# Kernel optimization log

Measured on AMD Instinct MI355X. Metric: run time of the kernel, lower is better.

The kernel has to match this reference:

```python
import jax, jax.numpy as jnp
import numpy as np
from jax.scipy.special import logsumexp

B, T, V, E, H, K = 64, 512, 21128, 256, 512, 31


def setup_inputs() -> dict:
    key = jax.random.key(0)
    ks = jax.random.split(key, 32)
    s = 1.0 / np.sqrt(H)

    def u(k, shape):
        return jax.random.uniform(k, shape, jnp.float32, -s, s)

    inp = {
        "input_ids": jax.random.randint(ks[0], (B, T), 0, V),
        "labels": jax.random.randint(ks[1], (B, T), 0, K),
        "emb": jax.random.normal(ks[2], (V, E), jnp.float32) * 0.05,
    }
    i = 3
    for layer, insz in (("l0", E), ("l1", 2 * H)):
        for d in ("f", "b"):
            inp["w_ih_%s%s" % (layer, d)] = u(ks[i], (3 * H, insz)); i += 1
            inp["w_hh_%s%s" % (layer, d)] = u(ks[i], (3 * H, H)); i += 1
            inp["b_ih_%s%s" % (layer, d)] = u(ks[i], (3 * H,)); i += 1
            inp["b_hh_%s%s" % (layer, d)] = u(ks[i], (3 * H,)); i += 1
    inp["cls_w"] = u(ks[i], (K, 2 * H))
    inp["cls_b"] = u(ks[i + 1], (K,))
    inp["crf_start"] = jax.random.normal(ks[i + 2], (K,), jnp.float32) * 0.1
    inp["crf_end"] = jax.random.normal(ks[i + 3], (K,), jnp.float32) * 0.1
    inp["crf_trans"] = jax.random.normal(ks[i + 4], (K, K), jnp.float32) * 0.1
    return inp


def gru_dir(x, w_ih, w_hh, b_ih, b_hh, reverse):
    # x: [B, T, in]. PyTorch GRU gate math, gates ordered (r, z, n).
    xp = jnp.einsum('bti,gi->btg', x, w_ih) + b_ih  # [B, T, 3H] precomputed input gates
    if reverse:
        xp = xp[:, ::-1]
    h0 = jnp.zeros((x.shape[0], w_hh.shape[1]), x.dtype)

    def step(h, xt):
        gh = h @ w_hh.T + b_hh
        xr, xz, xn = jnp.split(xt, 3, axis=-1)
        hr, hz, hn = jnp.split(gh, 3, axis=-1)
        r = jax.nn.sigmoid(xr + hr)
        z = jax.nn.sigmoid(xz + hz)
        n = jnp.tanh(xn + r * hn)
        h_new = (1.0 - z) * n + z * h
        return h_new, h_new

    _, hs = jax.lax.scan(step, h0, jnp.swapaxes(xp, 0, 1))
    hs = jnp.swapaxes(hs, 0, 1)  # [B, T, H]
    if reverse:
        hs = hs[:, ::-1]
    return hs


def crf_llh(emissions, tags, mask, start, end, trans):
    # Linear-chain CRF log-likelihood, summed over batch. mask[:, 0] assumed True.
    Bn = emissions.shape[0]
    mf = mask.astype(emissions.dtype)
    bidx = jnp.arange(Bn)
    em_t = jnp.take_along_axis(emissions, tags[:, :, None], axis=2)[:, :, 0]  # [B, T]
    num = start[tags[:, 0]] + em_t[:, 0]
    tr = trans[tags[:, :-1], tags[:, 1:]]  # [B, T-1]
    num = num + jnp.sum((tr + em_t[:, 1:]) * mf[:, 1:], axis=1)
    last_idx = jnp.sum(mask.astype(jnp.int32), axis=1) - 1
    num = num + end[tags[bidx, last_idx]]

    alpha0 = start[None, :] + emissions[:, 0]  # [B, K]

    def step(alpha, inp):
        em, m = inp  # em [B, K], m [B]
        nxt = logsumexp(alpha[:, :, None] + trans[None] + em[:, None, :], axis=1)
        return jnp.where(m[:, None], nxt, alpha), None

    alpha, _ = jax.lax.scan(
        step, alpha0,
        (jnp.swapaxes(emissions[:, 1:], 0, 1), jnp.swapaxes(mask[:, 1:], 0, 1)))
    denom = logsumexp(alpha + end[None, :], axis=1)
    return jnp.sum(num - denom)


def reference(input_ids, labels, emb,
              w_ih_l0f, w_hh_l0f, b_ih_l0f, b_hh_l0f,
              w_ih_l0b, w_hh_l0b, b_ih_l0b, b_hh_l0b,
              w_ih_l1f, w_hh_l1f, b_ih_l1f, b_hh_l1f,
              w_ih_l1b, w_hh_l1b, b_ih_l1b, b_hh_l1b,
              cls_w, cls_b, crf_start, crf_end, crf_trans):
    x = emb[input_ids]  # [B, T, E]
    f0 = gru_dir(x, w_ih_l0f, w_hh_l0f, b_ih_l0f, b_hh_l0f, False)
    b0 = gru_dir(x, w_ih_l0b, w_hh_l0b, b_ih_l0b, b_hh_l0b, True)
    h1 = jnp.concatenate([f0, b0], axis=-1)  # [B, T, 2H]
    f1 = gru_dir(h1, w_ih_l1f, w_hh_l1f, b_ih_l1f, b_hh_l1f, False)
    b1 = gru_dir(h1, w_ih_l1b, w_hh_l1b, b_ih_l1b, b_hh_l1b, True)
    gru_out = jnp.concatenate([f1, b1], axis=-1)  # [B, T, 2H]
    emissions = jnp.einsum('bth,kh->btk', gru_out, cls_w) + cls_b  # [B, T, K]
    mask = labels > -1  # labels.gt(labels_padding_value=-1)
    loss = -crf_llh(emissions, labels, mask, crf_start, crf_end, crf_trans)
    return (loss, emissions)
```

## Files before the change

kernel.cpp:

```cpp
#include <hip/hip_runtime.h>

#define DI __device__ __forceinline__

constexpr int B_  = 64;
constexpr int T_  = 512;
constexpr int E_  = 256;
constexpr int H_  = 512;
constexpr int G_  = 1536;
constexpr int H2_ = 1024;
constexpr int K_  = 31;
constexpr int BT_ = B_ * T_;
constexpr int TC_ = 64;
constexpr int NC_ = T_ / TC_;

typedef float        f32x4  __attribute__((ext_vector_type(4)));
typedef short        bf16x8 __attribute__((ext_vector_type(8)));
typedef unsigned int u32x4  __attribute__((ext_vector_type(4)));
typedef unsigned long long ull;

DI float bf2f(unsigned short u) {
    union { unsigned int i; float f; } v; v.i = ((unsigned int)u) << 16; return v.f;
}
DI unsigned short f2bf(float f) {
    union { float f; unsigned int i; } v; v.f = f;
    unsigned int r = v.i + 0x7fffu + ((v.i >> 16) & 1u);
    return (unsigned short)(r >> 16);
}
DI float sigm(float x) { return 1.f / (1.f + __expf(-x)); }
DI float tanh_(float x) {
    x = fminf(15.f, fmaxf(-15.f, x));
    float e = __expf(-2.f * x);
    return (1.f - e) / (1.f + e);
}

#define MFMA16(a, b, c) __builtin_amdgcn_mfma_f32_16x16x32_bf16(a, b, c, 0, 0, 0)

__global__ __launch_bounds__(256) void cvt_cls(const float* __restrict__ src,
                                               unsigned short* __restrict__ dstf,
                                               unsigned short* __restrict__ dstb) {
    int i = blockIdx.x * 256 + threadIdx.x;
    if (i >= 32 * H_) return;
    int n = i >> 9, k = i & 511;
    float vf = (n < K_) ? src[n * H2_ + k] : 0.f;
    float vb = (n < K_) ? src[n * H2_ + H_ + k] : 0.f;
    dstf[i] = f2bf(vf);
    dstb[i] = f2bf(vb);
}

__global__ __launch_bounds__(256) void emis_bias_init(const float* __restrict__ cls_b,
                                                      float* __restrict__ out1) {
    int i = blockIdx.x * 256 + threadIdx.x;
    int stride = gridDim.x * 256;
    for (; i < BT_ * K_; i += stride) {
        int n = i - (i / K_) * K_;
        out1[i] = cls_b[n];
    }
}

template <bool OUTF32, bool ACCUM, bool WF32, bool AGATHER>
DI void gemm_tile(unsigned short (*As)[40], unsigned short (*Ws)[40],
                  const unsigned short* A, const float* gsrc, const int* ids, int lda,
                  size_t arow0, const void* W, int ldw, int nrows, int n0,
                  const float* bias, void* Cout, int ldc, size_t crow0,
                  int nout, int ksz, int tid) {
    const int w = tid >> 6, l = tid & 63;
    const int srow = tid >> 2, sc8 = (tid & 3) * 8;
    const int mw = (w >> 1) * 32, nw = (w & 1) * 32;
    const int fl = l & 15, fk = (l >> 4) * 8;
    f32x4 z4 = { 0.f, 0.f, 0.f, 0.f };
    f32x4 acc[2][2];
    acc[0][0] = z4; acc[0][1] = z4; acc[1][0] = z4; acc[1][1] = z4;
    size_t abase;
    if (AGATHER) abase = (size_t)ids[arow0 + srow] * lda;
    else         abase = (arow0 + srow) * (size_t)lda;

    for (int kc = 0; kc < ksz; kc += 32) {
        u32x4 av, wvv;
        if (AGATHER) {
            const float4* ap = (const float4*)(gsrc + abase + kc + sc8);
            float4 a0 = ap[0], a1 = ap[1];
            union { unsigned short s[8]; u32x4 v; } r;
            r.s[0] = f2bf(a0.x); r.s[1] = f2bf(a0.y); r.s[2] = f2bf(a0.z); r.s[3] = f2bf(a0.w);
            r.s[4] = f2bf(a1.x); r.s[5] = f2bf(a1.y); r.s[6] = f2bf(a1.z); r.s[7] = f2bf(a1.w);
            av = r.v;
        } else {
            av = *(const u32x4*)(A + abase + kc + sc8);
        }
        if (WF32) {
            const float4* wp = (const float4*)((const float*)W + (size_t)(n0 + srow) * ldw + kc + sc8);
            float4 w0 = wp[0], w1 = wp[1];
            union { unsigned short s[8]; u32x4 v; } r;
            r.s[0] = f2bf(w0.x); r.s[1] = f2bf(w0.y); r.s[2] = f2bf(w0.z); r.s[3] = f2bf(w0.w);
            r.s[4] = f2bf(w1.x); r.s[5] = f2bf(w1.y); r.s[6] = f2bf(w1.z); r.s[7] = f2bf(w1.w);
            wvv = r.v;
        } else {
            if (n0 + srow < nrows)
                wvv = *(const u32x4*)((const unsigned short*)W + (size_t)(n0 + srow) * ldw + kc + sc8);
            else { u32x4 zz = { 0u, 0u, 0u, 0u }; wvv = zz; }
        }
        __syncthreads();
        *(u32x4*)&As[srow][sc8] = av;
        *(u32x4*)&Ws[srow][sc8] = wvv;
        __syncthreads();
        bf16x8 a0 = *(const bf16x8*)&As[mw + fl][fk];
        bf16x8 a1 = *(const bf16x8*)&As[mw + 16 + fl][fk];
        bf16x8 b0 = *(const bf16x8*)&Ws[nw + fl][fk];
        bf16x8 b1 = *(const bf16x8*)&Ws[nw + 16 + fl][fk];
        acc[0][0] = MFMA16(a0, b0, acc[0][0]);
        acc[0][1] = MFMA16(a0, b1, acc[0][1]);
        acc[1][0] = MFMA16(a1, b0, acc[1][0]);
        acc[1][1] = MFMA16(a1, b1, acc[1][1]);
    }

    #pragma unroll
    for (int mf = 0; mf < 2; ++mf)
        #pragma unroll
        for (int nf = 0; nf < 2; ++nf) {
            int col = n0 + nw + nf * 16 + fl;
            if (col >= nout) continue;
            float bv = bias ? bias[col] : 0.f;
            #pragma unroll
            for (int j = 0; j < 4; ++j) {
                int r = mw + mf * 16 + (l >> 4) * 4 + j;
                size_t crow = crow0 + r;
                float v = acc[mf][nf][j] + bv;
                if (OUTF32) {
                    float* C = (float*)Cout;
                    if (ACCUM) C[crow * ldc + col] += v;
                    else       C[crow * ldc + col] = v;
                } else {
                    ((unsigned short*)Cout)[crow * ldc + col] = f2bf(v);
                }
            }
        }
}

template <bool OUTF32, bool ACCUM, bool WF32, bool AGATHER>
__global__ __launch_bounds__(256) void gemm_k(
        const unsigned short* __restrict__ A, const float* __restrict__ gsrc,
        const int* __restrict__ ids, int lda, int m_base, int astride,
        const void* __restrict__ W, int ldw, int nrows,
        const float* __restrict__ bias,
        void* __restrict__ Cout, int ldc, int c_base, int cstride, int nout, int ksz) {
    __shared__ unsigned short As[64][40];
    __shared__ unsigned short Ws[64][40];
    gemm_tile<OUTF32, ACCUM, WF32, AGATHER>(As, Ws, A, gsrc, ids, lda,
        (size_t)m_base + (size_t)blockIdx.x * astride, W, ldw, nrows,
        blockIdx.y * 64, bias, Cout, ldc,
        (size_t)c_base + (size_t)blockIdx.x * cstride, nout, ksz, threadIdx.x);
}

template <bool AGATHER>
__global__ __launch_bounds__(256, 1) void fused_scan_gemm(
        int c, int layer,
        const unsigned short* __restrict__ xpc_f, const unsigned short* __restrict__ xpc_b,
        const float* __restrict__ whh_f, const float* __restrict__ whh_b,
        const float* __restrict__ bhh_f, const float* __restrict__ bhh_b,
        unsigned int* __restrict__ hpub,
        float* __restrict__ hcar,
        unsigned short* __restrict__ out_f, unsigned short* __restrict__ out_b,
        int ldo, int mode, int* __restrict__ flags,
        const unsigned short* __restrict__ gA, const float* __restrict__ gsrc,
        const int* __restrict__ gids, int glda,
        const float* __restrict__ gwf, const float* __restrict__ gwb,
        const float* __restrict__ gbf, const float* __restrict__ gbb,
        unsigned short* __restrict__ xpf_nxt, unsigned short* __restrict__ xpb_nxt,
        int t0f_n, int t0b_n, int do_gemm) {
    __shared__ unsigned short As[64][40];
    __shared__ unsigned short Ws[64][40];
    __shared__ unsigned short hs[16 * 512];
    const int bid = blockIdx.x;
    const int tid = threadIdx.x;

    if (bid >= 64) {
        if (!do_gemm) return;
        const int gb = bid - 64;
        for (int job = gb; job < 2 * 64 * 24; job += 192) {
            int dirj = job & 1;
            int rest = job >> 1;
            int mt = rest & 63;
            int nt = rest >> 6;
            const float* gw = dirj ? gwb : gwf;
            const float* gbias = dirj ? gbb : gbf;
            unsigned short* gout = dirj ? xpb_nxt : xpf_nxt;
            int t0 = dirj ? t0b_n : t0f_n;
            gemm_tile<false, false, true, AGATHER>(As, Ws, gA, gsrc, gids, glda,
                (size_t)t0 + (size_t)mt * T_, gw, glda, G_, nt * 64, gbias,
                (void*)gout, G_, (size_t)mt * TC_, G_, glda, tid);
        }
        return;
    }

    const int dir = bid >> 5;
    const int rb  = bid & 31;
    const int ug  = rb >> 2;
    const int bg  = rb & 3;
    const int w = tid >> 6, l = tid & 63;
    const int fl = l & 15, q = l >> 4, fko = q * 8;
    const unsigned short* xp = dir ? xpc_b : xpc_f;
    const float* whh = dir ? whh_b : whh_f;
    const float* bhh = dir ? bhh_b : bhh_f;
    unsigned short* outp = dir ? out_b : out_f;
    int* pollb  = flags + (dir * 4 + bg) * 8 * 32;
    int* myflag = pollb + ug * 32;

    const int u0w = ug * 64 + w * 16;
    bf16x8 wv[3][16];
    #pragma unroll
    for (int g = 0; g < 3; ++g)
        #pragma unroll
        for (int ks = 0; ks < 16; ++ks) {
            const float* wp = whh + (size_t)(g * H_ + u0w + fl) * H_ + ks * 32 + fko;
            float4 w0 = *(const float4*)wp, w1 = *(const float4*)(wp + 4);
            union { unsigned short s[8]; bf16x8 v; } r;
            r.s[0] = f2bf(w0.x); r.s[1] = f2bf(w0.y); r.s[2] = f2bf(w0.z); r.s[3] = f2bf(w0.w);
            r.s[4] = f2bf(w1.x); r.s[5] = f2bf(w1.y); r.s[6] = f2bf(w1.z); r.s[7] = f2bf(w1.w);
            wv[g][ks] = r.v;
        }

    const int u = u0w + fl;
    const float br_ = bhh[u], bz_ = bhh[H_ + u], bn_ = bhh[2 * H_ + u];
    const int mb = bg * 16 + q * 4;
    const int srowl = tid >> 4;
    const int sseg  = tid & 15;

    float hp[4];
    if (c > 0) {
        #pragma unroll
        for (int j = 0; j < 4; ++j) hp[j] = hcar[dir * (B_ * H_) + (mb + j) * H_ + u];
    } else {
        #pragma unroll
        for (int j = 0; j < 4; ++j) hp[j] = 0.f;
    }

    unsigned short xg[3][4];
    auto ldxp = [&](int tl) {
        #pragma unroll
        for (int j = 0; j < 4; ++j) {
            const unsigned short* xb = xp + ((size_t)((mb + j) * TC_ + tl) * G_) + u;
            xg[0][j] = xb[0]; xg[1][j] = xb[H_]; xg[2][j] = xb[2 * H_];
        }
    };
    ldxp(dir ? (TC_ - 1) : 0);

    for (int sl = 0; sl < TC_; ++sl) {
        const int s  = c * TC_ + sl;
        const int gs = layer * T_ + s;
        const int t = dir ? (T_ - 1 - s) : s;
        const int tloc = dir ? (TC_ - 1 - sl) : sl;

        f32x4 z4 = { 0.f, 0.f, 0.f, 0.f };
        f32x4 acc[3];
        acc[0] = z4; acc[1] = z4; acc[2] = z4;

        if (s > 0) {
            if (sl > 0) {
                int v = gs;
                if (l < 8) v = __hip_atomic_load(pollb + l * 32, __ATOMIC_RELAXED, __HIP_MEMORY_SCOPE_AGENT);
                while (!__all(v >= gs)) {
                    __builtin_amdgcn_s_sleep(1);
                    if (l < 8) v = __hip_atomic_load(pollb + l * 32, __ATOMIC_RELAXED, __HIP_MEMORY_SCOPE_AGENT);
                }
                asm volatile("" ::: "memory");
            }
            {
                const ull* src = (const ull*)(hpub
                    + ((size_t)((((s - 1) & 1) * 2 + dir) * B_ + bg * 16 + srowl)) * 256)
                    + sseg * 8;
                ull qv[8];
                #pragma unroll
                for (int i = 0; i < 8; ++i)
                    qv[i] = __hip_atomic_load(src + i, __ATOMIC_RELAXED, __HIP_MEMORY_SCOPE_AGENT);
                char* dst = (char*)hs + srowl * 1024;
                #pragma unroll
                for (int i = 0; i < 4; ++i) {
                    unsigned int byt = (unsigned int)(sseg * 64 + i * 16);
                    byt ^= ((unsigned int)(srowl & 7)) << 4;
                    union { ull qq[2]; u32x4 v4; } pk;
                    pk.qq[0] = qv[2 * i]; pk.qq[1] = qv[2 * i + 1];
                    *(u32x4*)(dst + byt) = pk.v4;
                }
            }
            __syncthreads();
            #pragma unroll
            for (int ks = 0; ks < 16; ++ks) {
                unsigned int byt = (unsigned int)(ks * 64 + q * 16);
                byt ^= ((unsigned int)(fl & 7)) << 4;
                bf16x8 afr = *(const bf16x8*)((const char*)hs + fl * 1024 + byt);
                acc[0] = MFMA16(afr, wv[0][ks], acc[0]);
                acc[1] = MFMA16(afr, wv[1][ks], acc[1]);
                acc[2] = MFMA16(afr, wv[2][ks], acc[2]);
            }
        }

        unsigned short hb16s[4];
        #pragma unroll
        for (int j = 0; j < 4; ++j) {
            float xr = bf2f(xg[0][j]);
            float xz = bf2f(xg[1][j]);
            float xn = bf2f(xg[2][j]);
            float r = sigm(xr + acc[0][j] + br_);
            float z = sigm(xz + acc[1][j] + bz_);
            float nn = tanh_(xn + r * (acc[2][j] + bn_));
            float hv = (1.f - z) * nn + z * hp[j];
            hp[j] = hv;
            hb16s[j] = f2bf(hv);
        }

        unsigned int* hw = hpub + (size_t)((s & 1) * 2 + dir) * (B_ * 256);
        #pragma unroll
        for (int j = 0; j < 4; ++j) {
            unsigned int pv = (unsigned int)(unsigned short)__shfl_xor((int)hb16s[j], 1);
            if ((fl & 1) == 0) {
                unsigned int pk32 = (unsigned int)hb16s[j] | (pv << 16);
                __hip_atomic_store(hw + (size_t)(mb + j) * 256 + (u >> 1), pk32,
                                   __ATOMIC_RELAXED, __HIP_MEMORY_SCOPE_AGENT);
            }
        }
        asm volatile("s_waitcnt vmcnt(0)" ::: "memory");
        __syncthreads();
        if (tid == 0)
            __hip_atomic_store(myflag, gs + 1, __ATOMIC_RELAXED, __HIP_MEMORY_SCOPE_AGENT);

        #pragma unroll
        for (int j = 0; j < 4; ++j) {
            size_t row = mode ? (size_t)((mb + j) * TC_ + tloc) : ((size_t)(mb + j) * T_ + t);
            outp[row * ldo + u] = hb16s[j];
        }
        if (sl < TC_ - 1) ldxp(dir ? (TC_ - 2 - sl) : (sl + 1));
    }

    #pragma unroll
    for (int j = 0; j < 4; ++j) hcar[dir * (B_ * H_) + (mb + j) * H_ + u] = hp[j];
}

__global__ __launch_bounds__(64) void crf_kernel(const float* __restrict__ em,
                                                 const int* __restrict__ labels,
                                                 const float* __restrict__ start,
                                                 const float* __restrict__ endv,
                                                 const float* __restrict__ trans,
                                                 float* __restrict__ partials) {
    __shared__ float tr[32 * 32];
    const int b = blockIdx.x, l = threadIdx.x;
    for (int e2 = l; e2 < 961; e2 += 64) {
        int r = e2 / 31, cc = e2 - r * 31;
        tr[r * 32 + cc] = trans[e2];
    }
    if (l < 32) tr[31 * 32 + l] = 0.f;
    __syncthreads();
    const int* lab = labels + b * T_;
    const float* eb = em + (size_t)b * T_ * K_;

    float part = 0.f, cnt = 0.f;
    for (int t = l; t < T_; t += 64) {
        int lt = lab[t];
        if (lt > -1) {
            cnt += 1.f;
            if (t > 0) part += tr[lab[t - 1] * 32 + lt] + eb[t * K_ + lt];
        }
    }
    #pragma unroll
    for (int o = 32; o; o >>= 1) { part += __shfl_xor(part, o); cnt += __shfl_xor(cnt, o); }
    int lastidx = (int)cnt - 1;
    float num = part + start[lab[0]] + eb[lab[0]] + endv[lab[lastidx]];

    const int jj = l & 31, half = l >> 5;
    const int i0 = half * 16;
    const int ecol = (jj < K_) ? jj : (K_ - 1);
    float a = (jj < K_) ? (start[jj] + eb[jj]) : -3.0e38f;
    for (int t = 1; t < T_; ++t) {
        float tv[16];
        float m = -3.0e38f;
        #pragma unroll
        for (int k = 0; k < 16; ++k) {
            float av = __shfl(a, i0 + k);
            float x = av + tr[(i0 + k) * 32 + jj];
            tv[k] = x;
            m = fmaxf(m, x);
        }
        float ss = 0.f;
        #pragma unroll
        for (int k = 0; k < 16; ++k) ss += __expf(tv[k] - m);
        float m2 = __shfl_xor(m, 32), s2 = __shfl_xor(ss, 32);
        float M = fmaxf(m, m2);
        float S = ss * __expf(m - M) + s2 * __expf(m2 - M);
        float anew = eb[t * K_ + ecol] + M + __logf(S);
        a = ((lab[t] > -1) && (jj < K_)) ? anew : a;
    }
    float v = (jj < K_) ? (a + endv[jj]) : -3.0e38f;
    float m = v;
    #pragma unroll
    for (int o = 32; o; o >>= 1) m = fmaxf(m, __shfl_xor(m, o));
    float ss = (half == 0 && jj < K_) ? __expf(v - m) : 0.f;
    #pragma unroll
    for (int o = 32; o; o >>= 1) ss += __shfl_xor(ss, o);
    if (l == 0) partials[b] = num - (m + __logf(ss));
}

__global__ __launch_bounds__(64) void loss_reduce(const float* __restrict__ partials,
                                                  float* __restrict__ out) {
    float v = partials[threadIdx.x];
    #pragma unroll
    for (int o = 32; o; o >>= 1) v += __shfl_xor(v, o);
    if (threadIdx.x == 0) out[0] = -v;
}

__global__ void sentinel(float* __restrict__ out, float v) { out[0] = -v; }

extern "C" void kernel_launch(void* const* d_in, const int* in_sizes, int n_in,
                              void* d_out, int out_size, void* d_ws, size_t ws_size,
                              hipStream_t stream) {
    const int*   ids      = (const int*)d_in[0];
    const int*   labels   = (const int*)d_in[1];
    const float* emb      = (const float*)d_in[2];
    const float* wih[4]   = { (const float*)d_in[3], (const float*)d_in[7], (const float*)d_in[11], (const float*)d_in[15] };
    const float* whh[4]   = { (const float*)d_in[4], (const float*)d_in[8], (const float*)d_in[12], (const float*)d_in[16] };
    const float* bih[4]   = { (const float*)d_in[5], (const float*)d_in[9], (const float*)d_in[13], (const float*)d_in[17] };
    const float* bhh[4]   = { (const float*)d_in[6], (const float*)d_in[10], (const float*)d_in[14], (const float*)d_in[18] };
    const float* cls_w    = (const float*)d_in[19];
    const float* cls_b    = (const float*)d_in[20];
    const float* c_start  = (const float*)d_in[21];
    const float* c_end    = (const float*)d_in[22];
    const float* c_trans  = (const float*)d_in[23];
    float* out = (float*)d_out;
    float* out1 = out + 1;

    char* p = (char*)d_ws;
    size_t used = 0;
    auto alloc = [&](size_t bytes) -> char* {
        char* r = p;
        size_t a = (bytes + 255) & ~(size_t)255;
        p += a; used += a;
        return r;
    };
    unsigned short* xpF[2]; unsigned short* xpB[2];
    for (int i = 0; i < 2; ++i) {
        xpF[i] = (unsigned short*)alloc((size_t)B_ * TC_ * G_ * 2);
        xpB[i] = (unsigned short*)alloc((size_t)B_ * TC_ * G_ * 2);
    }
    unsigned short* h1   = (unsigned short*)alloc((size_t)BT_ * H2_ * 2);
    unsigned short* gof  = (unsigned short*)alloc((size_t)B_ * TC_ * H_ * 2);
    unsigned short* gob  = (unsigned short*)alloc((size_t)B_ * TC_ * H_ * 2);
    unsigned short* clsf  = (unsigned short*)alloc((size_t)32 * H_ * 2);
    unsigned short* clshb = (unsigned short*)alloc((size_t)32 * H_ * 2);
    unsigned int*   hpub  = (unsigned int*)alloc((size_t)2 * 2 * B_ * 256 * 4);
    float*          hcar  = (float*)alloc((size_t)2 * B_ * H_ * 4);
    float*          partials = (float*)alloc((size_t)B_ * 4);
    int*            flags = (int*)alloc((size_t)2 * 4 * 8 * 32 * 4);

    if (used > ws_size) {
        sentinel<<<dim3(1), dim3(1), 0, stream>>>(out, (float)(ws_size >> 20));
        return;
    }

    hipMemsetAsync(flags, 0, (size_t)2 * 4 * 8 * 32 * 4, stream);
    cvt_cls<<<dim3((32 * H_ + 255) / 256), dim3(256), 0, stream>>>(cls_w, clsf, clshb);
    emis_bias_init<<<dim3(1024), dim3(256), 0, stream>>>(cls_b, out1);

    for (int layer = 0; layer < 2; ++layer) {
        const float* wf  = wih[layer * 2 + 0];
        const float* wb  = wih[layer * 2 + 1];
        const float* bf_ = bih[layer * 2 + 0];
        const float* bb_ = bih[layer * 2 + 1];
        const float* whf = whh[layer * 2 + 0];
        const float* whb = whh[layer * 2 + 1];
        const float* bhf = bhh[layer * 2 + 0];
        const float* bhb = bhh[layer * 2 + 1];

        if (layer == 0) {
            gemm_k<false, false, true, true><<<dim3(64, 24), dim3(256), 0, stream>>>(
                nullptr, emb, ids, E_, 0, T_, wf, E_, G_, bf_, (void*)xpF[0], G_, 0, TC_, G_, E_);
            gemm_k<false, false, true, true><<<dim3(64, 24), dim3(256), 0, stream>>>(
                nullptr, emb, ids, E_, T_ - TC_, T_, wb, E_, G_, bb_, (void*)xpB[0], G_, 0, TC_, G_, E_);
        } else {
            gemm_k<false, false, true, false><<<dim3(64, 24), dim3(256), 0, stream>>>(
                h1, nullptr, nullptr, H2_, 0, T_, wf, H2_, G_, bf_, (void*)xpF[0], G_, 0, TC_, G_, H2_);
            gemm_k<false, false, true, false><<<dim3(64, 24), dim3(256), 0, stream>>>(
                h1, nullptr, nullptr, H2_, T_ - TC_, T_, wb, H2_, G_, bb_, (void*)xpB[0], G_, 0, TC_, G_, H2_);
        }

        for (int c = 0; c < NC_; ++c) {
            int dg = (c + 1 < NC_) ? 1 : 0;
            int t0f_n = (c + 1) * TC_;
            int t0b_n = T_ - (c + 2) * TC_;
            if (layer == 0) {
                fused_scan_gemm<true><<<dim3(256), dim3(256), 0, stream>>>(
                    c, 0, xpF[c & 1], xpB[c & 1], whf, whb, bhf, bhb, hpub, hcar,
                    h1, h1 + H_, H2_, 0, flags,
                    nullptr, emb, ids, E_, wf, wb, bf_, bb_,
                    xpF[(c + 1) & 1], xpB[(c + 1) & 1], t0f_n, t0b_n, dg);
            } else {
                fused_scan_gemm<false><<<dim3(256), dim3(256), 0, stream>>>(
                    c, 1, xpF[c & 1], xpB[c & 1], whf, whb, bhf, bhb, hpub, hcar,
                    gof, gob, H_, 1, flags,
                    h1, nullptr, nullptr, H2_, wf, wb, bf_, bb_,
                    xpF[(c + 1) & 1], xpB[(c + 1) & 1], t0f_n, t0b_n, dg);
                int t0f = c * TC_;
                int t0b = T_ - (c + 1) * TC_;
                gemm_k<true, true, false, false><<<dim3(64, 1), dim3(256), 0, stream>>>(
                    gof, nullptr, nullptr, H_, 0, TC_, clsf, H_, 32, nullptr,
                    (void*)out1, K_, t0f, T_, K_, H_);
                gemm_k<true, true, false, false><<<dim3(64, 1), dim3(256), 0, stream>>>(
                    gob, nullptr, nullptr, H_, 0, TC_, clshb, H_, 32, nullptr,
                    (void*)out1, K_, t0b, T_, K_, H_);
            }
        }
    }

    crf_kernel<<<dim3(B_), dim3(64), 0, stream>>>(out1, labels, c_start, c_end, c_trans, partials);
    loss_reduce<<<dim3(1), dim3(64), 0, stream>>>(partials, out);
}
```

Baseline: 4.572 ms.

## Tag published hidden states with step number and validate on load

Each published pair of bf16 hidden values is widened to 64 bits, with the step index stored in the upper 32 bits. Consumers issue the hidden-state loads before the flag poll completes, then check that every tag matches the expected step and re-load until it does. The aim is to overlap the data fetch with flag waiting and to shorten the critical path of cross-block synchronisation. The cost is double the publish traffic, and the flag polling is still kept. The GEMM side-job loop is also reordered so each block takes a contiguous range of 16 jobs, changing the tile order.

```diff
diff --git a/kernel.cpp b/kernel.cpp
--- a/kernel.cpp
+++ b/kernel.cpp
@@ -156,7 +156,7 @@
         const unsigned short* __restrict__ xpc_f, const unsigned short* __restrict__ xpc_b,
         const float* __restrict__ whh_f, const float* __restrict__ whh_b,
         const float* __restrict__ bhh_f, const float* __restrict__ bhh_b,
-        unsigned int* __restrict__ hpub,
+        ull* __restrict__ hpub,
         float* __restrict__ hcar,
         unsigned short* __restrict__ out_f, unsigned short* __restrict__ out_b,
         int ldo, int mode, int* __restrict__ flags,
@@ -175,11 +175,13 @@
     if (bid >= 64) {
         if (!do_gemm) return;
         const int gb = bid - 64;
-        for (int job = gb; job < 2 * 64 * 24; job += 192) {
-            int dirj = job & 1;
-            int rest = job >> 1;
-            int mt = rest & 63;
-            int nt = rest >> 6;
+        #pragma unroll 1
+        for (int it = 0; it < 16; ++it) {
+            int job = gb * 16 + it;
+            int dirj = job / 1536;
+            int r2 = job - dirj * 1536;
+            int nt = r2 >> 6;
+            int mt = r2 & 63;
             const float* gw = dirj ? gwb : gwf;
             const float* gbias = dirj ? gbb : gbf;
             unsigned short* gout = dirj ? xpb_nxt : xpf_nxt;
@@ -254,6 +256,14 @@
         acc[0] = z4; acc[1] = z4; acc[2] = z4;
 
         if (s > 0) {
+            const ull* src = hpub
+                + ((size_t)((((s - 1) & 1) * 2 + dir) * B_) + bg * 16 + srowl) * 256
+                + sseg * 16;
+            ull qv[16];
+            #pragma unroll
+            for (int i = 0; i < 16; ++i)
+                qv[i] = __hip_atomic_load(src + i, __ATOMIC_RELAXED, __HIP_MEMORY_SCOPE_AGENT);
+
             if (sl > 0) {
                 int v = gs;
                 if (l < 8) v = __hip_atomic_load(pollb + l * 32, __ATOMIC_RELAXED, __HIP_MEMORY_SCOPE_AGENT);
@@ -264,20 +274,30 @@
                 asm volatile("" ::: "memory");
             }
             {
-                const ull* src = (const ull*)(hpub
-                    + ((size_t)((((s - 1) & 1) * 2 + dir) * B_ + bg * 16 + srowl)) * 256)
-                    + sseg * 8;
-                ull qv[8];
+                const unsigned int want = (unsigned int)(gs - 1);
+                bool ok = true;
                 #pragma unroll
-                for (int i = 0; i < 8; ++i)
-                    qv[i] = __hip_atomic_load(src + i, __ATOMIC_RELAXED, __HIP_MEMORY_SCOPE_AGENT);
+                for (int i = 0; i < 16; ++i) ok = ok && ((unsigned int)(qv[i] >> 32) == want);
+                while (!__all(ok)) {
+                    #pragma unroll
+                    for (int i = 0; i < 16; ++i)
+                        qv[i] = __hip_atomic_load(src + i, __ATOMIC_RELAXED, __HIP_MEMORY_SCOPE_AGENT);
+                    ok = true;
+                    #pragma unroll
+                    for (int i = 0; i < 16; ++i) ok = ok && ((unsigned int)(qv[i] >> 32) == want);
+                }
+            }
+            {
                 char* dst = (char*)hs + srowl * 1024;
                 #pragma unroll
                 for (int i = 0; i < 4; ++i) {
                     unsigned int byt = (unsigned int)(sseg * 64 + i * 16);
                     byt ^= ((unsigned int)(srowl & 7)) << 4;
-                    union { ull qq[2]; u32x4 v4; } pk;
-                    pk.qq[0] = qv[2 * i]; pk.qq[1] = qv[2 * i + 1];
+                    union { unsigned int uu[4]; u32x4 v4; } pk;
+                    pk.uu[0] = (unsigned int)qv[4 * i];
+                    pk.uu[1] = (unsigned int)qv[4 * i + 1];
+                    pk.uu[2] = (unsigned int)qv[4 * i + 2];
+                    pk.uu[3] = (unsigned int)qv[4 * i + 3];
                     *(u32x4*)(dst + byt) = pk.v4;
                 }
             }
@@ -307,13 +327,14 @@
             hb16s[j] = f2bf(hv);
         }
 
-        unsigned int* hw = hpub + (size_t)((s & 1) * 2 + dir) * (B_ * 256);
+        const ull tagw = ((ull)(unsigned int)gs) << 32;
+        ull* hw = hpub + (size_t)((s & 1) * 2 + dir) * (B_ * 256);
         #pragma unroll
         for (int j = 0; j < 4; ++j) {
             unsigned int pv = (unsigned int)(unsigned short)__shfl_xor((int)hb16s[j], 1);
             if ((fl & 1) == 0) {
                 unsigned int pk32 = (unsigned int)hb16s[j] | (pv << 16);
-                __hip_atomic_store(hw + (size_t)(mb + j) * 256 + (u >> 1), pk32,
+                __hip_atomic_store(hw + (size_t)(mb + j) * 256 + (u >> 1), tagw | pk32,
                                    __ATOMIC_RELAXED, __HIP_MEMORY_SCOPE_AGENT);
             }
         }
@@ -443,7 +464,7 @@
     unsigned short* gob  = (unsigned short*)alloc((size_t)B_ * TC_ * H_ * 2);
     unsigned short* clsf  = (unsigned short*)alloc((size_t)32 * H_ * 2);
     unsigned short* clshb = (unsigned short*)alloc((size_t)32 * H_ * 2);
-    unsigned int*   hpub  = (unsigned int*)alloc((size_t)2 * 2 * B_ * 256 * 4);
+    ull*            hpub  = (ull*)alloc((size_t)2 * 2 * B_ * 256 * 8);
     float*          hcar  = (float*)alloc((size_t)2 * B_ * H_ * 4);
     float*          partials = (float*)alloc((size_t)B_ * 4);
     int*            flags = (int*)alloc((size_t)2 * 4 * 8 * 32 * 4);
```

Measured after the change: 6.388 ms. 39.7% more time.
